# Optimization experiments

Measured on AMD Instinct MI355X. Metric: run time of the kernel, lower is better.

Reference implementation:

```python
import jax, jax.numpy as jnp
import numpy as np

BIT_SHIFT = 8
H, W = 480, 640
N = 100000
C_IN, C_HID, C_OUT = 96, 576, 96


def setup_inputs() -> dict:
    key = jax.random.key(0)
    ks = jax.random.split(key, 12)
    # --- sparse 2D coordinates (unique active sites on an H x W grid) ---
    rng = np.random.default_rng(0)
    lin = rng.choice(H * W, size=N, replace=False)
    ys, xs = lin // W, lin % W
    grid = -np.ones((H, W), dtype=np.int32)
    grid[ys, xs] = np.arange(N, dtype=np.int32)
    # neighbor index for each of the 9 kernel offsets; -1 where no active neighbor
    nbr = np.empty((9, N), dtype=np.int32)
    k = 0
    for dy in (-1, 0, 1):
        for dx in (-1, 0, 1):
            yn, xn = ys + dy, xs + dx
            valid = (yn >= 0) & (yn < H) & (xn >= 0) & (xn < W)
            idx = grid[np.clip(yn, 0, H - 1), np.clip(xn, 0, W - 1)]
            nbr[k] = np.where(valid, idx, -1)
            k += 1
    # --- int8-valued float features / weights (quantized integer inference) ---
    feats = jnp.round(jnp.clip(30.0 * jax.random.normal(ks[0], (N, C_IN)), -127, 127))
    w1 = jnp.round(jnp.clip(40.0 * jax.random.normal(ks[1], (C_IN, C_HID)), -127, 127))
    b1 = jnp.round(1000.0 * jax.random.normal(ks[2], (C_HID,)))
    w2 = jnp.round(jnp.clip(40.0 * jax.random.normal(ks[3], (9, C_HID)), -127, 127))
    b2 = jnp.round(1000.0 * jax.random.normal(ks[4], (C_HID,)))
    w3 = jnp.round(jnp.clip(40.0 * jax.random.normal(ks[5], (C_HID, C_OUT)), -127, 127))
    b3 = jnp.round(1000.0 * jax.random.normal(ks[6], (C_OUT,)))
    # per-output-channel requantization scaling factors (>= ~1 so round() is nonzero)
    s1 = 1.0 + 3.0 * jax.random.uniform(ks[7], (C_HID,))
    s2 = 1.0 + 3.0 * jax.random.uniform(ks[8], (C_HID,))
    s3 = 1.0 + 3.0 * jax.random.uniform(ks[9], (C_OUT,))
    s_main = 1.0 + 2.0 * jax.random.uniform(ks[10], ())
    s_res = 1.0 + 2.0 * jax.random.uniform(ks[11], ())
    return {"feats": feats, "neighbor_idx": jnp.asarray(nbr), "w1": w1, "b1": b1,
            "w2": w2, "b2": b2, "w3": w3, "b3": b3,
            "s1": s1, "s2": s2, "s3": s3, "s_main": s_main, "s_res": s_res}


def _requant(acc, s):
    # fused integer rescale: multiplier m = round(s) * 2^bit_shift, then /2^(2*bit_shift)
    B = 2.0 ** BIT_SHIFT
    return acc * (jnp.round(s) * B) / (B * B)


def _clamp(x):
    lim = 2.0 ** (BIT_SHIFT - 1)
    return jnp.clip(x, -lim, lim)


def _relu6(x):
    return jnp.clip(x, 0.0, 6.0)


def reference(feats, neighbor_idx, w1, b1, w2, b2, w3, b3, s1, s2, s3, s_main, s_res):
    B = 2.0 ** BIT_SHIFT
    # 1x1 expand conv (dense GEMM over active sites)
    x = _relu6(_clamp(_requant(feats @ w1 + b1, s1)))  # [N, C_HID]
    # depthwise 3x3 sparse conv: gather 9 neighbor taps, mask missing sites
    mask = (neighbor_idx >= 0).astype(x.dtype)               # [9, N]
    gathered = x[jnp.clip(neighbor_idx, 0, None)] * mask[:, :, None]  # [9, N, C_HID]
    dw = jnp.einsum('knc,kc->nc', gathered, w2) + b2
    x = _relu6(_clamp(_requant(dw, s2)))
    # 1x1 project conv
    x = _clamp(_requant(x @ w3 + b3, s3))                    # [N, C_OUT]
    # scaled residual add
    out = jnp.round(s_main) * B * x + jnp.round(s_res) * B * feats
    return out
```

## Files before the change

kernel.cpp:

```cpp
#include <hip/hip_runtime.h>
#include <hip/hip_bf16.h>
#include <hip/hip_fp16.h>

#define NS   100000
#define CIN  96
#define CHID 576
#define COUT 96
#define SPB  16
#define LDH  (CHID + 8)

typedef float    floatx4 __attribute__((ext_vector_type(4)));
typedef int      intx4   __attribute__((ext_vector_type(4)));
typedef short    short8  __attribute__((ext_vector_type(8)));
typedef _Float16 half8   __attribute__((ext_vector_type(8)));
typedef _Float16 half4   __attribute__((ext_vector_type(4)));

__global__ void prep_kernel(const float* __restrict__ w1, const float* __restrict__ w3,
                            const float* __restrict__ w2,
                            unsigned short* __restrict__ w1T, _Float16* __restrict__ w3T,
                            _Float16* __restrict__ w2h, _Float16* __restrict__ x1h) {
  int i = blockIdx.x * blockDim.x + threadIdx.x;
  if (i >= CHID * CIN) return;
  if (i < CHID) x1h[(size_t)NS * CHID + i] = (_Float16)0.0f;
  if (i < 9 * CHID) w2h[i] = (_Float16)w2[i];
  {
    int h = i / CIN, k = i % CIN;
    w1T[i] = (unsigned short)(__float_as_uint(w1[k * CHID + h]) >> 16);
  }
  {
    int o = i / CHID, k = i % CHID;
    w3T[i] = (_Float16)w3[k * COUT + o];
  }
}

__global__ __launch_bounds__(64) void expand_kernel(
    const float* __restrict__ feats, const float* __restrict__ b1,
    const float* __restrict__ s1, const unsigned short* __restrict__ w1T,
    _Float16* __restrict__ x1h) {
  const int lane = threadIdx.x;
  const int m = lane & 15, quad = lane >> 4;
  const int s0 = blockIdx.x * 64;

  short8 bfrag[4][3];
#pragma unroll
  for (int u = 0; u < 4; ++u) {
    const int site = min(s0 + u * 16 + m, NS - 1);
    const float* frow = feats + (size_t)site * CIN + quad * 8;
#pragma unroll
    for (int kc = 0; kc < 3; ++kc) {
      const float4 lo = *reinterpret_cast<const float4*>(frow + kc * 32);
      const float4 hi = *reinterpret_cast<const float4*>(frow + kc * 32 + 4);
      const float v[8] = {lo.x, lo.y, lo.z, lo.w, hi.x, hi.y, hi.z, hi.w};
#pragma unroll
      for (int j = 0; j < 8; ++j)
        bfrag[u][kc][j] = (short)(__float_as_uint(v[j]) >> 16);
    }
  }

  const int hq = quad * 4;
#pragma unroll 2
  for (int ht = 0; ht < CHID / 16; ++ht) {
    const unsigned short* wrow = w1T + (ht * 16 + m) * CIN + quad * 8;
    short8 a[3];
#pragma unroll
    for (int kc = 0; kc < 3; ++kc)
      a[kc] = *reinterpret_cast<const short8*>(wrow + kc * 32);

    floatx4 acc[4] = {{0.f, 0.f, 0.f, 0.f}, {0.f, 0.f, 0.f, 0.f},
                      {0.f, 0.f, 0.f, 0.f}, {0.f, 0.f, 0.f, 0.f}};
#pragma unroll
    for (int kc = 0; kc < 3; ++kc)
#pragma unroll
      for (int u = 0; u < 4; ++u)
        acc[u] = __builtin_amdgcn_mfma_f32_16x16x32_bf16(a[kc], bfrag[u][kc], acc[u], 0, 0, 0);

    const floatx4 bv = *reinterpret_cast<const floatx4*>(b1 + ht * 16 + hq);
    const floatx4 sv = *reinterpret_cast<const floatx4*>(s1 + ht * 16 + hq);
    floatx4 sc;
#pragma unroll
    for (int j = 0; j < 4; ++j) sc[j] = rintf(sv[j]) * (1.0f / 256.0f);

#pragma unroll
    for (int u = 0; u < 4; ++u) {
      const int site = s0 + u * 16 + m;
      if (site < NS) {
        half4 r;
#pragma unroll
        for (int j = 0; j < 4; ++j) {
          float v = (acc[u][j] + bv[j]) * sc[j];
          r[j] = (_Float16)fminf(fmaxf(v, 0.0f), 6.0f);
        }
        *reinterpret_cast<half4*>(x1h + (size_t)site * CHID + ht * 16 + hq) = r;
      }
    }
  }
}

__global__ __launch_bounds__(256) void dwproj_kernel(
    const int* __restrict__ nbr, const _Float16* __restrict__ w2h,
    const float* __restrict__ b2, const float* __restrict__ s2,
    const _Float16* __restrict__ x1h, const _Float16* __restrict__ w3T,
    const float* __restrict__ feats, const float* __restrict__ b3,
    const float* __restrict__ s3, const float* __restrict__ s_main,
    const float* __restrict__ s_res, float* __restrict__ out) {
  __shared__ _Float16 x2t[SPB * LDH];
  __shared__ _Float16 w2s[9 * CHID];
  __shared__ int offt[SPB * 12];
  const int t = threadIdx.x;
  const int s0 = blockIdx.x * SPB;

  if (t < SPB * 9) {
    const int k = t >> 4, n = t & 15;
    const int site = s0 + n;
    const int idx = nbr[k * NS + site];
    offt[n * 12 + k] = (idx < 0 ? NS : idx) * CHID;
  }
  for (int j = t; j < 9 * CHID / 8; j += 256)
    *reinterpret_cast<half8*>(w2s + j * 8) =
        *reinterpret_cast<const half8*>(w2h + j * 8);
  __syncthreads();

#pragma unroll 1
  for (int i = 0; i < 5; ++i) {
    const int w = i * 256 + t;
    if (w < SPB * 72) {
      const int n = w / 72, g = w - n * 72;
      const int c0 = g * 8;
      const intx4 oa = *reinterpret_cast<const intx4*>(offt + n * 12);
      const intx4 ob = *reinterpret_cast<const intx4*>(offt + n * 12 + 4);
      const int o8 = offt[n * 12 + 8];
      half8 v0 = *reinterpret_cast<const half8*>(x1h + (size_t)oa.x + c0);
      half8 v1 = *reinterpret_cast<const half8*>(x1h + (size_t)oa.y + c0);
      half8 v2 = *reinterpret_cast<const half8*>(x1h + (size_t)oa.z + c0);
      half8 v3 = *reinterpret_cast<const half8*>(x1h + (size_t)oa.w + c0);
      half8 v4 = *reinterpret_cast<const half8*>(x1h + (size_t)ob.x + c0);
      half8 v5 = *reinterpret_cast<const half8*>(x1h + (size_t)ob.y + c0);
      half8 v6 = *reinterpret_cast<const half8*>(x1h + (size_t)ob.z + c0);
      half8 v7 = *reinterpret_cast<const half8*>(x1h + (size_t)ob.w + c0);
      half8 v8 = *reinterpret_cast<const half8*>(x1h + (size_t)o8 + c0);
      float acc[8], scv[8];
      {
        const floatx4 ba = *reinterpret_cast<const floatx4*>(b2 + c0);
        const floatx4 bb = *reinterpret_cast<const floatx4*>(b2 + c0 + 4);
        const floatx4 sa = *reinterpret_cast<const floatx4*>(s2 + c0);
        const floatx4 sb = *reinterpret_cast<const floatx4*>(s2 + c0 + 4);
#pragma unroll
        for (int j = 0; j < 4; ++j) {
          acc[j] = ba[j];  acc[j + 4] = bb[j];
          scv[j] = rintf(sa[j]) * (1.0f / 256.0f);
          scv[j + 4] = rintf(sb[j]) * (1.0f / 256.0f);
        }
      }
      const half8 w0 = *reinterpret_cast<const half8*>(w2s + 0 * CHID + c0);
      const half8 w1v = *reinterpret_cast<const half8*>(w2s + 1 * CHID + c0);
      const half8 w2v = *reinterpret_cast<const half8*>(w2s + 2 * CHID + c0);
      const half8 w3v = *reinterpret_cast<const half8*>(w2s + 3 * CHID + c0);
      const half8 w4v = *reinterpret_cast<const half8*>(w2s + 4 * CHID + c0);
      const half8 w5v = *reinterpret_cast<const half8*>(w2s + 5 * CHID + c0);
      const half8 w6v = *reinterpret_cast<const half8*>(w2s + 6 * CHID + c0);
      const half8 w7v = *reinterpret_cast<const half8*>(w2s + 7 * CHID + c0);
      const half8 w8v = *reinterpret_cast<const half8*>(w2s + 8 * CHID + c0);
#pragma unroll
      for (int j = 0; j < 8; ++j) {
        acc[j] += (float)v0[j] * (float)w0[j];
        acc[j] += (float)v1[j] * (float)w1v[j];
        acc[j] += (float)v2[j] * (float)w2v[j];
        acc[j] += (float)v3[j] * (float)w3v[j];
        acc[j] += (float)v4[j] * (float)w4v[j];
        acc[j] += (float)v5[j] * (float)w5v[j];
        acc[j] += (float)v6[j] * (float)w6v[j];
        acc[j] += (float)v7[j] * (float)w7v[j];
        acc[j] += (float)v8[j] * (float)w8v[j];
      }
      half8 r;
#pragma unroll
      for (int j = 0; j < 8; ++j) {
        float v = acc[j] * scv[j];
        r[j] = (_Float16)fminf(fmaxf(v, 0.0f), 6.0f);
      }
      *reinterpret_cast<half8*>(x2t + n * LDH + c0) = r;
    }
  }
  __syncthreads();

  const int wave = t >> 6, lane = t & 63;
  const int m = lane & 15, quad = lane >> 4;
  const float rsm = rintf(s_main[0]) * 256.0f;
  const float rsr = rintf(s_res[0]) * 256.0f;

  for (int tile = wave; tile < (SPB / 16) * (COUT / 16); tile += 4) {
    const int tm = tile / (COUT / 16);
    const int ot = tile % (COUT / 16);
    floatx4 acc = {0.f, 0.f, 0.f, 0.f};
    const _Float16* arow = w3T + (ot * 16 + m) * CHID + quad * 8;
    const _Float16* blds = x2t + (tm * 16 + m) * LDH + quad * 8;
#pragma unroll
    for (int kc = 0; kc < 18; ++kc) {
      const half8 a = *reinterpret_cast<const half8*>(arow + kc * 32);
      const half8 b = *reinterpret_cast<const half8*>(blds + kc * 32);
      acc = __builtin_amdgcn_mfma_f32_16x16x32_f16(a, b, acc, 0, 0, 0);
    }
    const int site = s0 + tm * 16 + m;
    if (site < NS) {
      const int o0 = ot * 16 + quad * 4;
      const floatx4 b3v = *reinterpret_cast<const floatx4*>(b3 + o0);
      const floatx4 s3v = *reinterpret_cast<const floatx4*>(s3 + o0);
      const floatx4 fv =
          *reinterpret_cast<const floatx4*>(feats + (size_t)site * COUT + o0);
      floatx4 r;
#pragma unroll
      for (int j = 0; j < 4; ++j) {
        float v = (acc[j] + b3v[j]) * (rintf(s3v[j]) * (1.0f / 256.0f));
        v = fminf(fmaxf(v, -128.0f), 128.0f);
        r[j] = rsm * v + rsr * fv[j];
      }
      *reinterpret_cast<floatx4*>(out + (size_t)site * COUT + o0) = r;
    }
  }
}

extern "C" void kernel_launch(void* const* d_in, const int* in_sizes, int n_in,
                              void* d_out, int out_size, void* d_ws, size_t ws_size,
                              hipStream_t stream) {
  const float* feats  = (const float*)d_in[0];
  const int*   nbr    = (const int*)d_in[1];
  const float* w1     = (const float*)d_in[2];
  const float* b1     = (const float*)d_in[3];
  const float* w2     = (const float*)d_in[4];
  const float* b2     = (const float*)d_in[5];
  const float* w3     = (const float*)d_in[6];
  const float* b3     = (const float*)d_in[7];
  const float* s1     = (const float*)d_in[8];
  const float* s2     = (const float*)d_in[9];
  const float* s3     = (const float*)d_in[10];
  const float* s_main = (const float*)d_in[11];
  const float* s_res  = (const float*)d_in[12];
  float* out = (float*)d_out;

  char* ws = (char*)d_ws;
  _Float16*       x1h = (_Float16*)ws;
  unsigned short* w1T = (unsigned short*)(ws + 115201152);
  _Float16*       w3T = (_Float16*)(ws + 115311744);
  _Float16*       w2h = (_Float16*)(ws + 115422336);

  prep_kernel<<<(CHID * CIN + 255) / 256, 256, 0, stream>>>(w1, w3, w2, w1T, w3T, w2h, x1h);
  expand_kernel<<<(NS + 63) / 64, 64, 0, stream>>>(feats, b1, s1, w1T, x1h);
  const int nblk = (NS + SPB - 1) / SPB;
  dwproj_kernel<<<nblk, 256, 0, stream>>>(nbr, w2h, b2, s2, x1h, w3T,
                                          feats, b3, s3, s_main, s_res, out);
}
```

Before: 296.2 us.

## Double the sites per block and software-pipeline depthwise neighbor gathers

Each block now handles 32 sites instead of 16, which doubles the shared-memory tile and cuts the number of blocks. The depthwise stage becomes a software pipeline: the next iteration's nine neighbor loads, bias and scale are issued before the current iteration's FMAs, so gather latency overlaps with compute. The block covers 2304 work items in exactly 9 iterations of 256 threads, so the bounds check is gone. This costs more registers (two sets of nine half8 values), which may lower occupancy, and the larger LDS tile may also reduce blocks per CU.

Result: slower. 316.6 us (+6.9%).

```diff
diff --git a/kernel.cpp b/kernel.cpp
--- a/kernel.cpp
+++ b/kernel.cpp
@@ -6,7 +6,7 @@
 #define CIN  96
 #define CHID 576
 #define COUT 96
-#define SPB  16
+#define SPB  32
 #define LDH  (CHID + 8)
 
 typedef float    floatx4 __attribute__((ext_vector_type(4)));
@@ -109,10 +109,9 @@
   const int t = threadIdx.x;
   const int s0 = blockIdx.x * SPB;
 
-  if (t < SPB * 9) {
-    const int k = t >> 4, n = t & 15;
-    const int site = s0 + n;
-    const int idx = nbr[k * NS + site];
+  for (int j = t; j < SPB * 9; j += 256) {
+    const int k = j >> 5, n = j & 31;
+    const int idx = nbr[k * NS + s0 + n];
     offt[n * 12 + k] = (idx < 0 ? NS : idx) * CHID;
   }
   for (int j = t; j < 9 * CHID / 8; j += 256)
@@ -120,57 +119,84 @@
         *reinterpret_cast<const half8*>(w2h + j * 8);
   __syncthreads();
 
+  {
+    half8 cur[9], nxt[9];
+    floatx4 cb0, cb1, cs0, cs1, nb0, nb1, ns0, ns1;
+    {
+      const int w = t;
+      const int n = w / 72, g = w - (w / 72) * 72, c0 = g * 8;
+      const int* op = offt + n * 12;
+      const intx4 oa = *reinterpret_cast<const intx4*>(op);
+      const intx4 ob = *reinterpret_cast<const intx4*>(op + 4);
+      const int o8 = op[8];
+      cur[0] = *reinterpret_cast<const half8*>(x1h + (size_t)oa.x + c0);
+      cur[1] = *reinterpret_cast<const half8*>(x1h + (size_t)oa.y + c0);
+      cur[2] = *reinterpret_cast<const half8*>(x1h + (size_t)oa.z + c0);
+      cur[3] = *reinterpret_cast<const half8*>(x1h + (size_t)oa.w + c0);
+      cur[4] = *reinterpret_cast<const half8*>(x1h + (size_t)ob.x + c0);
+      cur[5] = *reinterpret_cast<const half8*>(x1h + (size_t)ob.y + c0);
+      cur[6] = *reinterpret_cast<const half8*>(x1h + (size_t)ob.z + c0);
+      cur[7] = *reinterpret_cast<const half8*>(x1h + (size_t)ob.w + c0);
+      cur[8] = *reinterpret_cast<const half8*>(x1h + (size_t)o8 + c0);
+      cb0 = *reinterpret_cast<const floatx4*>(b2 + c0);
+      cb1 = *reinterpret_cast<const floatx4*>(b2 + c0 + 4);
+      cs0 = *reinterpret_cast<const floatx4*>(s2 + c0);
+      cs1 = *reinterpret_cast<const floatx4*>(s2 + c0 + 4);
+    }
 #pragma unroll 1
-  for (int i = 0; i < 5; ++i) {
-    const int w = i * 256 + t;
-    if (w < SPB * 72) {
-      const int n = w / 72, g = w - n * 72;
-      const int c0 = g * 8;
-      const intx4 oa = *reinterpret_cast<const intx4*>(offt + n * 12);
-      const intx4 ob = *reinterpret_cast<const intx4*>(offt + n * 12 + 4);
-      const int o8 = offt[n * 12 + 8];
-      half8 v0 = *reinterpret_cast<const half8*>(x1h + (size_t)oa.x + c0);
-      half8 v1 = *reinterpret_cast<const half8*>(x1h + (size_t)oa.y + c0);
-      half8 v2 = *reinterpret_cast<const half8*>(x1h + (size_t)oa.z + c0);
-      half8 v3 = *reinterpret_cast<const half8*>(x1h + (size_t)oa.w + c0);
-      half8 v4 = *reinterpret_cast<const half8*>(x1h + (size_t)ob.x + c0);
-      half8 v5 = *reinterpret_cast<const half8*>(x1h + (size_t)ob.y + c0);
-      half8 v6 = *reinterpret_cast<const half8*>(x1h + (size_t)ob.z + c0);
-      half8 v7 = *reinterpret_cast<const half8*>(x1h + (size_t)ob.w + c0);
-      half8 v8 = *reinterpret_cast<const half8*>(x1h + (size_t)o8 + c0);
+    for (int i = 0; i < 9; ++i) {
+      const int w = i * 256 + t;
+      const int n = w / 72, g = w - (w / 72) * 72, c0 = g * 8;
+      if (i < 8) {
+        const int w2_ = w + 256;
+        const int n2 = w2_ / 72, g2 = w2_ - (w2_ / 72) * 72, c2 = g2 * 8;
+        const int* op = offt + n2 * 12;
+        const intx4 oa = *reinterpret_cast<const intx4*>(op);
+        const intx4 ob = *reinterpret_cast<const intx4*>(op + 4);
+        const int o8 = op[8];
+        nxt[0] = *reinterpret_cast<const half8*>(x1h + (size_t)oa.x + c2);
+        nxt[1] = *reinterpret_cast<const half8*>(x1h + (size_t)oa.y + c2);
+        nxt[2] = *reinterpret_cast<const half8*>(x1h + (size_t)oa.z + c2);
+        nxt[3] = *reinterpret_cast<const half8*>(x1h + (size_t)oa.w + c2);
+        nxt[4] = *reinterpret_cast<const half8*>(x1h + (size_t)ob.x + c2);
+        nxt[5] = *reinterpret_cast<const half8*>(x1h + (size_t)ob.y + c2);
+        nxt[6] = *reinterpret_cast<const half8*>(x1h + (size_t)ob.z + c2);
+        nxt[7] = *reinterpret_cast<const half8*>(x1h + (size_t)ob.w + c2);
+        nxt[8] = *reinterpret_cast<const half8*>(x1h + (size_t)o8 + c2);
+        nb0 = *reinterpret_cast<const floatx4*>(b2 + c2);
+        nb1 = *reinterpret_cast<const floatx4*>(b2 + c2 + 4);
+        ns0 = *reinterpret_cast<const floatx4*>(s2 + c2);
+        ns1 = *reinterpret_cast<const floatx4*>(s2 + c2 + 4);
+      }
       float acc[8], scv[8];
+#pragma unroll
+      for (int j = 0; j < 4; ++j) {
+        acc[j] = cb0[j];  acc[j + 4] = cb1[j];
+        scv[j] = rintf(cs0[j]) * (1.0f / 256.0f);
+        scv[j + 4] = rintf(cs1[j]) * (1.0f / 256.0f);
+      }
       {
-        const floatx4 ba = *reinterpret_cast<const floatx4*>(b2 + c0);
-        const floatx4 bb = *reinterpret_cast<const floatx4*>(b2 + c0 + 4);
-        const floatx4 sa = *reinterpret_cast<const floatx4*>(s2 + c0);
-        const floatx4 sb = *reinterpret_cast<const floatx4*>(s2 + c0 + 4);
-#pragma unroll
-        for (int j = 0; j < 4; ++j) {
-          acc[j] = ba[j];  acc[j + 4] = bb[j];
-          scv[j] = rintf(sa[j]) * (1.0f / 256.0f);
-          scv[j + 4] = rintf(sb[j]) * (1.0f / 256.0f);
+        const half8 w0 = *reinterpret_cast<const half8*>(w2s + 0 * CHID + c0);
+        const half8 w1v = *reinterpret_cast<const half8*>(w2s + 1 * CHID + c0);
+        const half8 w2v = *reinterpret_cast<const half8*>(w2s + 2 * CHID + c0);
+        const half8 w3v = *reinterpret_cast<const half8*>(w2s + 3 * CHID + c0);
+        const half8 w4v = *reinterpret_cast<const half8*>(w2s + 4 * CHID + c0);
+        const half8 w5v = *reinterpret_cast<const half8*>(w2s + 5 * CHID + c0);
+        const half8 w6v = *reinterpret_cast<const half8*>(w2s + 6 * CHID + c0);
+        const half8 w7v = *reinterpret_cast<const half8*>(w2s + 7 * CHID + c0);
+        const half8 w8v = *reinterpret_cast<const half8*>(w2s + 8 * CHID + c0);
+#pragma unroll
+        for (int j = 0; j < 8; ++j) {
+          acc[j] += (float)cur[0][j] * (float)w0[j];
+          acc[j] += (float)cur[1][j] * (float)w1v[j];
+          acc[j] += (float)cur[2][j] * (float)w2v[j];
+          acc[j] += (float)cur[3][j] * (float)w3v[j];
+          acc[j] += (float)cur[4][j] * (float)w4v[j];
+          acc[j] += (float)cur[5][j] * (float)w5v[j];
+          acc[j] += (float)cur[6][j] * (float)w6v[j];
+          acc[j] += (float)cur[7][j] * (float)w7v[j];
+          acc[j] += (float)cur[8][j] * (float)w8v[j];
         }
-      }
-      const half8 w0 = *reinterpret_cast<const half8*>(w2s + 0 * CHID + c0);
-      const half8 w1v = *reinterpret_cast<const half8*>(w2s + 1 * CHID + c0);
-      const half8 w2v = *reinterpret_cast<const half8*>(w2s + 2 * CHID + c0);
-      const half8 w3v = *reinterpret_cast<const half8*>(w2s + 3 * CHID + c0);
-      const half8 w4v = *reinterpret_cast<const half8*>(w2s + 4 * CHID + c0);
-      const half8 w5v = *reinterpret_cast<const half8*>(w2s + 5 * CHID + c0);
-      const half8 w6v = *reinterpret_cast<const half8*>(w2s + 6 * CHID + c0);
-      const half8 w7v = *reinterpret_cast<const half8*>(w2s + 7 * CHID + c0);
-      const half8 w8v = *reinterpret_cast<const half8*>(w2s + 8 * CHID + c0);
-#pragma unroll
-      for (int j = 0; j < 8; ++j) {
-        acc[j] += (float)v0[j] * (float)w0[j];
-        acc[j] += (float)v1[j] * (float)w1v[j];
-        acc[j] += (float)v2[j] * (float)w2v[j];
-        acc[j] += (float)v3[j] * (float)w3v[j];
-        acc[j] += (float)v4[j] * (float)w4v[j];
-        acc[j] += (float)v5[j] * (float)w5v[j];
-        acc[j] += (float)v6[j] * (float)w6v[j];
-        acc[j] += (float)v7[j] * (float)w7v[j];
-        acc[j] += (float)v8[j] * (float)w8v[j];
       }
       half8 r;
 #pragma unroll
@@ -179,6 +205,11 @@
         r[j] = (_Float16)fminf(fmaxf(v, 0.0f), 6.0f);
       }
       *reinterpret_cast<half8*>(x2t + n * LDH + c0) = r;
+      if (i < 8) {
+#pragma unroll
+        for (int k = 0; k < 9; ++k) cur[k] = nxt[k];
+        cb0 = nb0; cb1 = nb1; cs0 = ns0; cs1 = ns1;
+      }
     }
   }
   __syncthreads();
```
